# Kernel tuning notes

Measured on AMD Instinct MI355X. Metric: run time of the kernel, lower is better.

Reference implementation:

```python
import jax, jax.numpy as jnp
import numpy as np

N = 100000          # nodes
E = 1600000         # edges (avg degree 16)
NUM_NODES = 100000  # embedding vocab
EMB = 128
HID = 64
G = 256             # graphs in the batch


def setup_inputs() -> dict:
    key = jax.random.key(0)
    ks = jax.random.split(key, 14)
    x_ids = jax.random.randint(ks[0], (N,), 0, NUM_NODES)
    edge_index = jax.random.randint(ks[1], (2, E), 0, N)
    batch = jnp.sort(jax.random.randint(ks[2], (N,), 0, G))
    s = 0.05
    emb = jax.random.normal(ks[3], (NUM_NODES, EMB), jnp.float32) * s
    W1 = jax.random.normal(ks[4], (EMB, HID), jnp.float32) * s
    b1 = jnp.zeros((HID,), jnp.float32)
    W2 = jax.random.normal(ks[5], (HID, HID), jnp.float32) * s
    b2 = jnp.zeros((HID,), jnp.float32)
    W3 = jax.random.normal(ks[6], (HID, HID), jnp.float32) * s
    b3 = jnp.zeros((HID,), jnp.float32)
    Wf1 = jax.random.normal(ks[7], (HID, HID), jnp.float32) * s
    bf1 = jnp.zeros((HID,), jnp.float32)
    Wf2 = jax.random.normal(ks[8], (HID, 1), jnp.float32) * s
    bf2 = jnp.zeros((1,), jnp.float32)
    return dict(x_ids=x_ids, edge_index=edge_index, batch=batch, emb=emb,
                W1=W1, b1=b1, W2=W2, b2=b2, W3=W3, b3=b3,
                Wf1=Wf1, bf1=bf1, Wf2=Wf2, bf2=bf2)


def gcn_conv(x, W, b, src, dst, num_nodes):
    # PyG GCNConv: x' = D^{-1/2} (A + I) D^{-1/2} (x W) + b
    xw = x @ W  # [N, out]
    ones = jnp.ones(src.shape[0], x.dtype)
    deg = jax.ops.segment_sum(ones, dst, num_segments=num_nodes) + 1.0  # self-loop
    dinv = jax.lax.rsqrt(deg)
    coef = dinv[src] * dinv[dst]  # per-edge norm
    agg = jax.ops.segment_sum(xw[src] * coef[:, None], dst, num_segments=num_nodes)
    agg = agg + xw * (dinv * dinv)[:, None]  # self-loop message
    return agg + b


def reference(x_ids, edge_index, batch, emb, W1, b1, W2, b2, W3, b3, Wf1, bf1, Wf2, bf2):
    src, dst = edge_index[0], edge_index[1]
    x = emb[x_ids]                                   # [N, EMB]
    x = jax.nn.relu(gcn_conv(x, W1, b1, src, dst, N))
    x = jax.nn.relu(gcn_conv(x, W2, b2, src, dst, N))
    x = jax.nn.relu(gcn_conv(x, W3, b3, src, dst, N))
    # global mean pool per graph
    counts = jax.ops.segment_sum(jnp.ones(N, x.dtype), batch, num_segments=G)
    pooled = jax.ops.segment_sum(x, batch, num_segments=G) / jnp.maximum(counts, 1.0)[:, None]
    h = jax.nn.relu(pooled @ Wf1 + bf1)
    out = (h @ Wf2 + bf2).squeeze(-1)                # [G]
    return jax.nn.sigmoid(out)
```

## Files before the change

### kernel.cpp

```cpp
#include <hip/hip_runtime.h>
#include <hip/hip_bf16.h>


typedef unsigned short u16;
typedef unsigned int u32;
typedef unsigned long long u64;

__device__ __forceinline__ float bf2f(u32 u) {
  return __uint_as_float(u << 16);
}
__device__ __forceinline__ u16 f2bf(float f) {
  u32 x = __float_as_uint(f);
  return (u16)((x + 0x7fffu + ((x >> 16) & 1u)) >> 16);
}

__global__ __launch_bounds__(256) void k_init(int4* __restrict__ csr4, long long n4,
                                              int* __restrict__ cnt, int n, int zb) {
  if ((int)blockIdx.x < zb) {
    long long i = (long long)blockIdx.x * blockDim.x + threadIdx.x;
    long long stride = (long long)zb * blockDim.x;
    int4 z = make_int4(0, 0, 0, 0);
    for (; i < n4; i += stride) csr4[i] = z;
  } else {
    int nb = gridDim.x - zb;
    int i = (blockIdx.x - zb) * blockDim.x + threadIdx.x;
    int stride = nb * blockDim.x;
    for (; i < n; i += stride) cnt[i] = 0;
  }
}

__global__ __launch_bounds__(256) void k_count_rank(const int* __restrict__ dst, int* __restrict__ cnt,
                                                    int* __restrict__ rank, int e_count) {
  int e = blockIdx.x * blockDim.x + threadIdx.x;
  if (e < e_count) rank[e] = atomicAdd(&cnt[dst[e]], 1);
}

__global__ __launch_bounds__(256) void k_scan1(const int* __restrict__ cnt, int n, int* __restrict__ bsum) {
  __shared__ int s[256];
  int b = blockIdx.x, t = threadIdx.x;
  int base = b * 1024;
  int sum = 0;
  #pragma unroll
  for (int i = 0; i < 4; ++i) {
    int idx = base + t + i * 256;
    if (idx < n) sum += (cnt[idx] + 7) & ~7;
  }
  s[t] = sum; __syncthreads();
  for (int off = 128; off > 0; off >>= 1) {
    if (t < off) s[t] += s[t + off];
    __syncthreads();
  }
  if (t == 0) bsum[b] = s[0];
}

__global__ __launch_bounds__(128) void k_scan2(int* __restrict__ bsum, int nb, int* __restrict__ total_out) {
  __shared__ int sh[128];
  int t = threadIdx.x;
  sh[t] = (t < nb) ? bsum[t] : 0;
  __syncthreads();
  for (int off = 1; off < 128; off <<= 1) {
    int x = sh[t];
    int y = (t >= off) ? sh[t - off] : 0;
    __syncthreads();
    sh[t] = x + y;
    __syncthreads();
  }
  if (t < nb) bsum[t] = (t == 0) ? 0 : sh[t - 1];
  if (t == 0) *total_out = sh[127];
}

__global__ __launch_bounds__(256) void k_scan3(const int* __restrict__ cnt, int n,
                                               const int* __restrict__ bsum_ex, int* __restrict__ offsets,
                                               float* __restrict__ dinv) {
  __shared__ int sh[256];
  int b = blockIdx.x, t = threadIdx.x;
  int base = b * 1024 + t * 4;
  int c0 = (base + 0 < n) ? cnt[base + 0] : 0;
  int c1 = (base + 1 < n) ? cnt[base + 1] : 0;
  int c2 = (base + 2 < n) ? cnt[base + 2] : 0;
  int c3 = (base + 3 < n) ? cnt[base + 3] : 0;
  if (base + 0 < n) dinv[base + 0] = rsqrtf((float)c0 + 1.0f);
  if (base + 1 < n) dinv[base + 1] = rsqrtf((float)c1 + 1.0f);
  if (base + 2 < n) dinv[base + 2] = rsqrtf((float)c2 + 1.0f);
  if (base + 3 < n) dinv[base + 3] = rsqrtf((float)c3 + 1.0f);
  int v0 = (c0 + 7) & ~7, v1 = (c1 + 7) & ~7, v2 = (c2 + 7) & ~7, v3 = (c3 + 7) & ~7;
  sh[t] = v0 + v1 + v2 + v3;
  __syncthreads();
  for (int off = 1; off < 256; off <<= 1) {
    int x = sh[t];
    int y = (t >= off) ? sh[t - off] : 0;
    __syncthreads();
    sh[t] = x + y;
    __syncthreads();
  }
  int run = bsum_ex[b] + ((t == 0) ? 0 : sh[t - 1]);
  if (base + 0 < n) offsets[base + 0] = run; run += v0;
  if (base + 1 < n) offsets[base + 1] = run; run += v1;
  if (base + 2 < n) offsets[base + 2] = run; run += v2;
  if (base + 3 < n) offsets[base + 3] = run;
}

__global__ __launch_bounds__(256, 4) void k_mm1_scatter(
    const int* __restrict__ ids, const float* __restrict__ emb,
    const float* __restrict__ W1, u16* __restrict__ out, int n, int mmb,
    const int* __restrict__ src, const int* __restrict__ dst,
    const int* __restrict__ rank, const float* __restrict__ dinv,
    const int* __restrict__ offs, long long* __restrict__ csr, int e_count) {
  if ((int)blockIdx.x >= mmb) {
    int e = (blockIdx.x - mmb) * 256 + threadIdx.x;
    if (e < e_count) {
      int s = src[e], d = dst[e];
      int pos = offs[d] + rank[e];
      u64 val = (u64)(u32)s | ((u64)(u32)__float_as_uint(dinv[s] * dinv[d]) << 32);
      __builtin_nontemporal_store((long long)val, &csr[pos]);
    }
    return;
  }

  const int lane = threadIdx.x & 63;
  const int w = threadIdx.x >> 6;
  const int r = blockIdx.x * 256 + w * 64 + lane;
  const int rid = ids[(r < n) ? r : (n - 1)];
  const float4* __restrict__ xrow = reinterpret_cast<const float4*>(emb + (size_t)rid * 128);

  float acc[64];
  #pragma unroll
  for (int j = 0; j < 64; ++j) acc[j] = 0.f;

  #pragma unroll 1
  for (int s = 0; s < 4; ++s) {
    float4 xb[8];
    #pragma unroll
    for (int i = 0; i < 8; ++i) xb[i] = xrow[s * 8 + i];
    const float* __restrict__ wbase = W1 + (size_t)(s * 32) * 64;
    #pragma unroll
    for (int i = 0; i < 8; ++i) {
      const float* __restrict__ w0 = wbase + (i * 4) * 64;
      #pragma unroll
      for (int j = 0; j < 64; ++j) {
        acc[j] = fmaf(xb[i].x, w0[j], acc[j]);
        acc[j] = fmaf(xb[i].y, w0[64 + j], acc[j]);
        acc[j] = fmaf(xb[i].z, w0[128 + j], acc[j]);
        acc[j] = fmaf(xb[i].w, w0[192 + j], acc[j]);
      }
    }
  }

  if (r < n) {
    u16* op = out + (size_t)r * 64;
    #pragma unroll
    for (int q = 0; q < 8; ++q) {
      uint2 pk;
      pk.x = ((u32)f2bf(acc[q * 4 + 1]) << 16) | f2bf(acc[q * 4 + 0]);
      pk.y = ((u32)f2bf(acc[q * 4 + 3]) << 16) | f2bf(acc[q * 4 + 2]);
      *reinterpret_cast<uint2*>(op + q * 4) = pk;
    }
  }
}


template <bool FINAL>
__global__ __launch_bounds__(256) void k_agg(const u16* __restrict__ xw, const int2* __restrict__ csr,
                                             const int* __restrict__ offs, const float* __restrict__ dinv,
                                             const float* __restrict__ bias, const float* __restrict__ Wn,
                                             u16* __restrict__ out, int n) {
  const int lane = threadIdx.x & 63;
  const int w = threadIdx.x >> 6;
  const float bl = bias[lane];
  const int ngroups = (n + 3) >> 2;
  const int nwaves = gridDim.x * 4;

  for (int grp = blockIdx.x * 4 + w; grp < ngroups; grp += nwaves) {
    const int v0 = grp * 4;
    const int c1 = (v0 + 1 < n) ? v0 + 1 : n;
    const int c2 = (v0 + 2 < n) ? v0 + 2 : n;
    const int c3 = (v0 + 3 < n) ? v0 + 3 : n;
    const int b0 = offs[v0], b1 = offs[c1], b2 = offs[c2], b3 = offs[c3];
    const int b4 = offs[(v0 + 4 < n) ? v0 + 4 : n];

    float d0 = dinv[v0];
    float d1 = dinv[(c1 < n) ? c1 : v0];
    float d2 = dinv[(c2 < n) ? c2 : v0];
    float d3 = dinv[(c3 < n) ? c3 : v0];
    float acc0 = fmaf(bf2f((u32)xw[(size_t)v0 * 64 + lane]), d0 * d0, bl);
    float acc1 = (c1 < n) ? fmaf(bf2f((u32)xw[(size_t)c1 * 64 + lane]), d1 * d1, bl) : 0.f;
    float acc2 = (c2 < n) ? fmaf(bf2f((u32)xw[(size_t)c2 * 64 + lane]), d2 * d2, bl) : 0.f;
    float acc3 = (c3 < n) ? fmaf(bf2f((u32)xw[(size_t)c3 * 64 + lane]), d3 * d3, bl) : 0.f;

    int e = b0;
    while (e < b4) {
      int cnt = b4 - e;
      cnt = (cnt < 64) ? cnt : 64;
      int cex, cey;
      {
        int2 ce = make_int2(0, 0);
        if (lane < cnt) ce = csr[e + lane];
        cex = ce.x; cey = ce.y;
      }
      for (int bs = 0; bs < cnt; bs += 8) {
        float vv[8];
        #pragma unroll
        for (int t = 0; t < 8; ++t) {
          int sb = __builtin_amdgcn_readlane(cex, bs + t);
          vv[t] = bf2f((u32)xw[(size_t)sb * 64 + lane]);
        }
        float tmp = 0.f;
        #pragma unroll
        for (int t = 0; t < 8; ++t) {
          float cf = __int_as_float(__builtin_amdgcn_readlane(cey, bs + t));
          tmp = fmaf(vv[t], cf, tmp);
        }
        const int ep = e + bs;
        if (ep < b1) acc0 += tmp;
        else if (ep < b2) acc1 += tmp;
        else if (ep < b3) acc2 += tmp;
        else acc3 += tmp;
      }
      e += cnt;
    }

    float h0 = fmaxf(acc0, 0.f), h1 = fmaxf(acc1, 0.f);
    float h2 = fmaxf(acc2, 0.f), h3 = fmaxf(acc3, 0.f);
    if constexpr (FINAL) {
      out[(size_t)v0 * 64 + lane] = f2bf(h0);
      if (c1 < n) out[(size_t)c1 * 64 + lane] = f2bf(h1);
      if (c2 < n) out[(size_t)c2 * 64 + lane] = f2bf(h2);
      if (c3 < n) out[(size_t)c3 * 64 + lane] = f2bf(h3);
    } else {
      const int hb0 = __float_as_int(h0), hb1 = __float_as_int(h1);
      const int hb2 = __float_as_int(h2), hb3 = __float_as_int(h3);
      float o0 = 0.f, o1 = 0.f, o2 = 0.f, o3 = 0.f;
      #pragma unroll
      for (int k = 0; k < 64; ++k) {
        float wk = Wn[k * 64 + lane];
        o0 = fmaf(__int_as_float(__builtin_amdgcn_readlane(hb0, k)), wk, o0);
        o1 = fmaf(__int_as_float(__builtin_amdgcn_readlane(hb1, k)), wk, o1);
        o2 = fmaf(__int_as_float(__builtin_amdgcn_readlane(hb2, k)), wk, o2);
        o3 = fmaf(__int_as_float(__builtin_amdgcn_readlane(hb3, k)), wk, o3);
      }
      out[(size_t)v0 * 64 + lane] = f2bf(o0);
      if (c1 < n) out[(size_t)c1 * 64 + lane] = f2bf(o1);
      if (c2 < n) out[(size_t)c2 * 64 + lane] = f2bf(o2);
      if (c3 < n) out[(size_t)c3 * 64 + lane] = f2bf(o3);
    }
  }
}

__global__ __launch_bounds__(256) void k_pool(const u16* __restrict__ x, const int* __restrict__ batch, int n,
                                              const float* __restrict__ Wf1, const float* __restrict__ bf1,
                                              const float* __restrict__ Wf2, const float* __restrict__ bf2,
                                              float* __restrict__ out) {
  int g = blockIdx.x;
  int tid = threadIdx.x, lane = tid & 63, w = tid >> 6;
  int a = 0, b = n;
  while (a < b) { int m = (a + b) >> 1; if (batch[m] < g) a = m + 1; else b = m; }
  int lo = a;
  b = n;
  while (a < b) { int m = (a + b) >> 1; if (batch[m] < g + 1) a = m + 1; else b = m; }
  int hi = a;

  float acc = 0.f;
  for (int r = lo + w; r < hi; r += 4) acc += bf2f((u32)x[(size_t)r * 64 + lane]);
  __shared__ float red[4][64];
  __shared__ float mean[64];
  red[w][lane] = acc;
  __syncthreads();
  if (w == 0) {
    float s = red[0][lane] + red[1][lane] + red[2][lane] + red[3][lane];
    mean[lane] = s / fmaxf((float)(hi - lo), 1.0f);
  }
  __syncthreads();
  if (w == 0) {
    float h = bf1[lane];
    #pragma unroll
    for (int k = 0; k < 64; ++k) h = fmaf(mean[k], Wf1[k * 64 + lane], h);
    h = fmaxf(h, 0.f);
    float vv = h * Wf2[lane];
    for (int off = 32; off > 0; off >>= 1) vv += __shfl_down(vv, off, 64);
    if (lane == 0) out[g] = 1.0f / (1.0f + expf(-(vv + bf2[0])));
  }
}

static inline char* align256(char* p) {
  return (char*)(((uintptr_t)p + 255) & ~(uintptr_t)255);
}

extern "C" void kernel_launch(void* const* d_in, const int* in_sizes, int n_in,
                              void* d_out, int out_size, void* d_ws, size_t ws_size,
                              hipStream_t stream) {
  const int*   x_ids = (const int*)d_in[0];
  const int*   edge  = (const int*)d_in[1];
  const int*   batch = (const int*)d_in[2];
  const float* emb   = (const float*)d_in[3];
  const float* W1    = (const float*)d_in[4];
  const float* b1    = (const float*)d_in[5];
  const float* W2    = (const float*)d_in[6];
  const float* b2    = (const float*)d_in[7];
  const float* W3    = (const float*)d_in[8];
  const float* b3    = (const float*)d_in[9];
  const float* Wf1   = (const float*)d_in[10];
  const float* bf1   = (const float*)d_in[11];
  const float* Wf2   = (const float*)d_in[12];
  const float* bf2   = (const float*)d_in[13];
  float* out = (float*)d_out;

  const int N = in_sizes[0];
  const int E = in_sizes[1] / 2;
  const int G = out_size;
  const int* e_src = edge;
  const int* e_dst = edge + E;

  const size_t EPAD = (size_t)E + 8 * (size_t)(N + 1) + 64;

  char* p = (char*)d_ws;
  u16*   bufA = (u16*)p;              p = align256(p + (size_t)N * 64 * 2);
  u16*   bufB = (u16*)p;              p = align256(p + (size_t)N * 64 * 2);
  int2*  csr  = (int2*)p;             p = align256(p + EPAD * 8);
  int*   rank = (int*)p;              p = align256(p + (size_t)E * 4);
  float* dinv = (float*)p;            p = align256(p + (size_t)N * 4);
  int*   cnt  = (int*)p;              p = align256(p + (size_t)N * 4);
  int*   offs = (int*)p;              p = align256(p + (size_t)(N + 1) * 4);
  int*   bsum = (int*)p;              p = align256(p + (size_t)1024 * 4);
  (void)ws_size; (void)n_in;

  const int nb_scan = (N + 1023) / 1024;
  dim3 blk(256);

  k_init<<<dim3(1024 + 128), blk, 0, stream>>>((int4*)csr, (long long)(EPAD * 2 / 4), cnt, N, 1024);
  k_count_rank<<<dim3((E + 255) / 256), blk, 0, stream>>>(e_dst, cnt, rank, E);
  k_scan1<<<dim3(nb_scan), blk, 0, stream>>>(cnt, N, bsum);
  k_scan2<<<dim3(1), dim3(128), 0, stream>>>(bsum, nb_scan, offs + N);
  k_scan3<<<dim3(nb_scan), blk, 0, stream>>>(cnt, N, bsum, offs, dinv);

  const int mmb = (N + 255) / 256;
  const int scb = (E + 255) / 256;
  k_mm1_scatter<<<dim3(mmb + scb), blk, 0, stream>>>(
      x_ids, emb, W1, bufA, N, mmb,
      e_src, e_dst, rank, dinv, offs, (long long*)csr, E);

  k_agg<false><<<dim3(2048), blk, 0, stream>>>(bufA, csr, offs, dinv, b1, W2, bufB, N);
  k_agg<false><<<dim3(2048), blk, 0, stream>>>(bufB, csr, offs, dinv, b2, W3, bufA, N);
  k_agg<true><<<dim3(2048), blk, 0, stream>>>(bufA, csr, offs, dinv, b3, nullptr, bufB, N);

  k_pool<<<dim3(G), blk, 0, stream>>>(bufB, batch, N, Wf1, bf1, Wf2, bf2, out);
}
```

Measured before the change: 399.0 us.

## Shrink CSR to source-only indices and split degree counters eight ways

Each CSR entry shrinks from an (src, coef) pair of 8 bytes to a 4-byte source index. Aggregation now gathers dinv[src] per edge and applies the destination's dinv once per 8-edge batch. Degree counting spreads atomics over 8 partitioned counter arrays, which the scans merge. Those scans also set per-partition scatter bases and fill only the padding slots with a dummy node whose dinv is zero, so the full CSR zero-fill disappears. The aim is less CSR traffic in all three aggregation passes, less atomic contention, and less initialization work. The cost is an extra dinv gather per edge, and padding now reads the never-written dummy row N of the feature buffers, which could inject NaNs.

```diff
diff --git a/kernel.cpp b/kernel.cpp
--- a/kernel.cpp
+++ b/kernel.cpp
@@ -4,7 +4,6 @@
 
 typedef unsigned short u16;
 typedef unsigned int u32;
-typedef unsigned long long u64;
 
 __device__ __forceinline__ float bf2f(u32 u) {
   return __uint_as_float(u << 16);
@@ -14,28 +13,22 @@
   return (u16)((x + 0x7fffu + ((x >> 16) & 1u)) >> 16);
 }
 
-__global__ __launch_bounds__(256) void k_init(int4* __restrict__ csr4, long long n4,
-                                              int* __restrict__ cnt, int n, int zb) {
-  if ((int)blockIdx.x < zb) {
-    long long i = (long long)blockIdx.x * blockDim.x + threadIdx.x;
-    long long stride = (long long)zb * blockDim.x;
-    int4 z = make_int4(0, 0, 0, 0);
-    for (; i < n4; i += stride) csr4[i] = z;
-  } else {
-    int nb = gridDim.x - zb;
-    int i = (blockIdx.x - zb) * blockDim.x + threadIdx.x;
-    int stride = nb * blockDim.x;
-    for (; i < n; i += stride) cnt[i] = 0;
-  }
-}
-
-__global__ __launch_bounds__(256) void k_count_rank(const int* __restrict__ dst, int* __restrict__ cnt,
-                                                    int* __restrict__ rank, int e_count) {
+__global__ __launch_bounds__(256) void k_init(int* __restrict__ cnt8, int n8) {
+  int i = blockIdx.x * blockDim.x + threadIdx.x;
+  int stride = gridDim.x * blockDim.x;
+  for (; i < n8; i += stride) cnt8[i] = 0;
+}
+
+__global__ __launch_bounds__(256) void k_count_rank(const int* __restrict__ dst, int* __restrict__ cnt8,
+                                                    int* __restrict__ rank, int e_count, int n) {
   int e = blockIdx.x * blockDim.x + threadIdx.x;
-  if (e < e_count) rank[e] = atomicAdd(&cnt[dst[e]], 1);
-}
-
-__global__ __launch_bounds__(256) void k_scan1(const int* __restrict__ cnt, int n, int* __restrict__ bsum) {
+  if (e < e_count) {
+    int p = blockIdx.x & 7;
+    rank[e] = atomicAdd(&cnt8[p * n + dst[e]], 1);
+  }
+}
+
+__global__ __launch_bounds__(256) void k_scan1(const int* __restrict__ cnt8, int n, int* __restrict__ bsum) {
   __shared__ int s[256];
   int b = blockIdx.x, t = threadIdx.x;
   int base = b * 1024;
@@ -43,7 +36,12 @@
   #pragma unroll
   for (int i = 0; i < 4; ++i) {
     int idx = base + t + i * 256;
-    if (idx < n) sum += (cnt[idx] + 7) & ~7;
+    if (idx < n) {
+      int c = 0;
+      #pragma unroll
+      for (int q = 0; q < 8; ++q) c += cnt8[q * n + idx];
+      sum += (c + 7) & ~7;
+    }
   }
   s[t] = sum; __syncthreads();
   for (int off = 128; off > 0; off >>= 1) {
@@ -69,22 +67,27 @@
   if (t == 0) *total_out = sh[127];
 }
 
-__global__ __launch_bounds__(256) void k_scan3(const int* __restrict__ cnt, int n,
+__global__ __launch_bounds__(256) void k_scan3(int* __restrict__ cnt8, int n,
                                                const int* __restrict__ bsum_ex, int* __restrict__ offsets,
-                                               float* __restrict__ dinv) {
+                                               float* __restrict__ dinv, u32* __restrict__ csr) {
   __shared__ int sh[256];
   int b = blockIdx.x, t = threadIdx.x;
   int base = b * 1024 + t * 4;
-  int c0 = (base + 0 < n) ? cnt[base + 0] : 0;
-  int c1 = (base + 1 < n) ? cnt[base + 1] : 0;
-  int c2 = (base + 2 < n) ? cnt[base + 2] : 0;
-  int c3 = (base + 3 < n) ? cnt[base + 3] : 0;
-  if (base + 0 < n) dinv[base + 0] = rsqrtf((float)c0 + 1.0f);
-  if (base + 1 < n) dinv[base + 1] = rsqrtf((float)c1 + 1.0f);
-  if (base + 2 < n) dinv[base + 2] = rsqrtf((float)c2 + 1.0f);
-  if (base + 3 < n) dinv[base + 3] = rsqrtf((float)c3 + 1.0f);
-  int v0 = (c0 + 7) & ~7, v1 = (c1 + 7) & ~7, v2 = (c2 + 7) & ~7, v3 = (c3 + 7) & ~7;
-  sh[t] = v0 + v1 + v2 + v3;
+  int cq[4][8];
+  int c[4], v[4];
+  #pragma unroll
+  for (int i = 0; i < 4; ++i) {
+    c[i] = 0;
+    #pragma unroll
+    for (int q = 0; q < 8; ++q) {
+      int x = (base + i < n) ? cnt8[q * n + base + i] : 0;
+      cq[i][q] = x;
+      c[i] += x;
+    }
+    v[i] = (c[i] + 7) & ~7;
+    if (base + i < n) dinv[base + i] = rsqrtf((float)c[i] + 1.0f);
+  }
+  sh[t] = v[0] + v[1] + v[2] + v[3];
   __syncthreads();
   for (int off = 1; off < 256; off <<= 1) {
     int x = sh[t];
@@ -94,25 +97,37 @@
     __syncthreads();
   }
   int run = bsum_ex[b] + ((t == 0) ? 0 : sh[t - 1]);
-  if (base + 0 < n) offsets[base + 0] = run; run += v0;
-  if (base + 1 < n) offsets[base + 1] = run; run += v1;
-  if (base + 2 < n) offsets[base + 2] = run; run += v2;
-  if (base + 3 < n) offsets[base + 3] = run;
+  #pragma unroll
+  for (int i = 0; i < 4; ++i) {
+    if (base + i < n) {
+      offsets[base + i] = run;
+      int pb = run;
+      #pragma unroll
+      for (int q = 0; q < 8; ++q) {
+        cnt8[q * n + base + i] = pb;
+        pb += cq[i][q];
+      }
+      for (int j = run + c[i]; j < run + v[i]; ++j) csr[j] = (u32)n;
+      run += v[i];
+    }
+  }
+  if (b == 0 && t == 0) dinv[n] = 0.f;
 }
 
 __global__ __launch_bounds__(256, 4) void k_mm1_scatter(
     const int* __restrict__ ids, const float* __restrict__ emb,
     const float* __restrict__ W1, u16* __restrict__ out, int n, int mmb,
     const int* __restrict__ src, const int* __restrict__ dst,
-    const int* __restrict__ rank, const float* __restrict__ dinv,
-    const int* __restrict__ offs, long long* __restrict__ csr, int e_count) {
+    const int* __restrict__ rank, const int* __restrict__ pbase,
+    u32* __restrict__ csr, int e_count) {
   if ((int)blockIdx.x >= mmb) {
-    int e = (blockIdx.x - mmb) * 256 + threadIdx.x;
+    int eb = blockIdx.x - mmb;
+    int e = eb * 256 + threadIdx.x;
     if (e < e_count) {
-      int s = src[e], d = dst[e];
-      int pos = offs[d] + rank[e];
-      u64 val = (u64)(u32)s | ((u64)(u32)__float_as_uint(dinv[s] * dinv[d]) << 32);
-      __builtin_nontemporal_store((long long)val, &csr[pos]);
+      int p = eb & 7;
+      int d = dst[e];
+      int pos = pbase[p * n + d] + rank[e];
+      __builtin_nontemporal_store((u32)src[e], &csr[pos]);
     }
     return;
   }
@@ -160,7 +175,7 @@
 
 
 template <bool FINAL>
-__global__ __launch_bounds__(256) void k_agg(const u16* __restrict__ xw, const int2* __restrict__ csr,
+__global__ __launch_bounds__(256) void k_agg(const u16* __restrict__ xw, const u32* __restrict__ csr,
                                              const int* __restrict__ offs, const float* __restrict__ dinv,
                                              const float* __restrict__ bias, const float* __restrict__ Wn,
                                              u16* __restrict__ out, int n) {
@@ -178,10 +193,10 @@
     const int b0 = offs[v0], b1 = offs[c1], b2 = offs[c2], b3 = offs[c3];
     const int b4 = offs[(v0 + 4 < n) ? v0 + 4 : n];
 
-    float d0 = dinv[v0];
-    float d1 = dinv[(c1 < n) ? c1 : v0];
-    float d2 = dinv[(c2 < n) ? c2 : v0];
-    float d3 = dinv[(c3 < n) ? c3 : v0];
+    const float d0 = dinv[v0];
+    const float d1 = dinv[(c1 < n) ? c1 : v0];
+    const float d2 = dinv[(c2 < n) ? c2 : v0];
+    const float d3 = dinv[(c3 < n) ? c3 : v0];
     float acc0 = fmaf(bf2f((u32)xw[(size_t)v0 * 64 + lane]), d0 * d0, bl);
     float acc1 = (c1 < n) ? fmaf(bf2f((u32)xw[(size_t)c1 * 64 + lane]), d1 * d1, bl) : 0.f;
     float acc2 = (c2 < n) ? fmaf(bf2f((u32)xw[(size_t)c2 * 64 + lane]), d2 * d2, bl) : 0.f;
@@ -189,34 +204,28 @@
 
     int e = b0;
     while (e < b4) {
-      int cnt = b4 - e;
-      cnt = (cnt < 64) ? cnt : 64;
-      int cex, cey;
-      {
-        int2 ce = make_int2(0, 0);
-        if (lane < cnt) ce = csr[e + lane];
-        cex = ce.x; cey = ce.y;
-      }
-      for (int bs = 0; bs < cnt; bs += 8) {
-        float vv[8];
+      int cc = b4 - e;
+      cc = (cc < 64) ? cc : 64;
+      u32 ce = (u32)n;
+      if (lane < cc) ce = csr[e + lane];
+      for (int bs = 0; bs < cc; bs += 8) {
+        float xv[8], dv[8];
         #pragma unroll
         for (int t = 0; t < 8; ++t) {
-          int sb = __builtin_amdgcn_readlane(cex, bs + t);
-          vv[t] = bf2f((u32)xw[(size_t)sb * 64 + lane]);
+          int sb = __builtin_amdgcn_readlane((int)ce, bs + t);
+          xv[t] = bf2f((u32)xw[(size_t)sb * 64 + lane]);
+          dv[t] = dinv[sb];
         }
         float tmp = 0.f;
         #pragma unroll
-        for (int t = 0; t < 8; ++t) {
-          float cf = __int_as_float(__builtin_amdgcn_readlane(cey, bs + t));
-          tmp = fmaf(vv[t], cf, tmp);
-        }
+        for (int t = 0; t < 8; ++t) tmp = fmaf(xv[t], dv[t], tmp);
         const int ep = e + bs;
-        if (ep < b1) acc0 += tmp;
-        else if (ep < b2) acc1 += tmp;
-        else if (ep < b3) acc2 += tmp;
-        else acc3 += tmp;
+        if (ep < b1) acc0 = fmaf(tmp, d0, acc0);
+        else if (ep < b2) acc1 = fmaf(tmp, d1, acc1);
+        else if (ep < b3) acc2 = fmaf(tmp, d2, acc2);
+        else acc3 = fmaf(tmp, d3, acc3);
       }
-      e += cnt;
+      e += cc;
     }
 
     float h0 = fmaxf(acc0, 0.f), h1 = fmaxf(acc1, 0.f);
@@ -313,12 +322,12 @@
   const size_t EPAD = (size_t)E + 8 * (size_t)(N + 1) + 64;
 
   char* p = (char*)d_ws;
-  u16*   bufA = (u16*)p;              p = align256(p + (size_t)N * 64 * 2);
-  u16*   bufB = (u16*)p;              p = align256(p + (size_t)N * 64 * 2);
-  int2*  csr  = (int2*)p;             p = align256(p + EPAD * 8);
+  u16*   bufA = (u16*)p;              p = align256(p + (size_t)(N + 1) * 64 * 2);
+  u16*   bufB = (u16*)p;              p = align256(p + (size_t)(N + 1) * 64 * 2);
+  u32*   csr  = (u32*)p;              p = align256(p + EPAD * 4);
   int*   rank = (int*)p;              p = align256(p + (size_t)E * 4);
-  float* dinv = (float*)p;            p = align256(p + (size_t)N * 4);
-  int*   cnt  = (int*)p;              p = align256(p + (size_t)N * 4);
+  float* dinv = (float*)p;            p = align256(p + (size_t)(N + 1) * 4);
+  int*   cnt8 = (int*)p;              p = align256(p + (size_t)8 * N * 4);
   int*   offs = (int*)p;              p = align256(p + (size_t)(N + 1) * 4);
   int*   bsum = (int*)p;              p = align256(p + (size_t)1024 * 4);
   (void)ws_size; (void)n_in;
@@ -326,17 +335,17 @@
   const int nb_scan = (N + 1023) / 1024;
   dim3 blk(256);
 
-  k_init<<<dim3(1024 + 128), blk, 0, stream>>>((int4*)csr, (long long)(EPAD * 2 / 4), cnt, N, 1024);
-  k_count_rank<<<dim3((E + 255) / 256), blk, 0, stream>>>(e_dst, cnt, rank, E);
-  k_scan1<<<dim3(nb_scan), blk, 0, stream>>>(cnt, N, bsum);
+  k_init<<<dim3(512), blk, 0, stream>>>(cnt8, 8 * N);
+  k_count_rank<<<dim3((E + 255) / 256), blk, 0, stream>>>(e_dst, cnt8, rank, E, N);
+  k_scan1<<<dim3(nb_scan), blk, 0, stream>>>(cnt8, N, bsum);
   k_scan2<<<dim3(1), dim3(128), 0, stream>>>(bsum, nb_scan, offs + N);
-  k_scan3<<<dim3(nb_scan), blk, 0, stream>>>(cnt, N, bsum, offs, dinv);
+  k_scan3<<<dim3(nb_scan), blk, 0, stream>>>(cnt8, N, bsum, offs, dinv, csr);
 
   const int mmb = (N + 255) / 256;
   const int scb = (E + 255) / 256;
   k_mm1_scatter<<<dim3(mmb + scb), blk, 0, stream>>>(
       x_ids, emb, W1, bufA, N, mmb,
-      e_src, e_dst, rank, dinv, offs, (long long*)csr, E);
+      e_src, e_dst, rank, cnt8, csr, E);
 
   k_agg<false><<<dim3(2048), blk, 0, stream>>>(bufA, csr, offs, dinv, b1, W2, bufB, N);
   k_agg<false><<<dim3(2048), blk, 0, stream>>>(bufB, csr, offs, dinv, b2, W3, bufA, N);
```

Result: no change. 399.9 us (+0.2%).
